# Kernel tuning notes

Measured on AMD Instinct MI355X. Metric: run time of the kernel, lower is better.

## Reference

```python
import jax, jax.numpy as jnp
import numpy as np


def setup_inputs() -> dict:
    key = jax.random.key(0)
    ks = jax.random.split(key, 8)
    B, Te, De, Dd, H = 64, 1024, 1024, 1024, 1024
    return {
        "encoder_outputs": jax.random.normal(ks[0], (B, Te, De), jnp.float32),
        "decoder_outputs": jax.random.normal(ks[1], (B, 1, Dd), jnp.float32),
        "Wa_w": jax.random.normal(ks[2], (H, Dd), jnp.float32) * 0.02,
        "Wa_b": jax.random.normal(ks[3], (H,), jnp.float32) * 0.02,
        "Ua_w": jax.random.normal(ks[4], (H, De), jnp.float32) * 0.02,
        "Ua_b": jax.random.normal(ks[5], (H,), jnp.float32) * 0.02,
        "Va_w": jax.random.normal(ks[6], (1, H), jnp.float32) * 0.02,
        "Va_b": jax.random.normal(ks[7], (1,), jnp.float32) * 0.02,
    }


def reference(encoder_outputs, decoder_outputs, Wa_w, Wa_b, Ua_w, Ua_b, Va_w, Va_b):
    # Wa: [B,1,H], Ua: [B,Te,H]  (torch Linear: x @ W.T + b)
    Wa = jnp.einsum('bqd,hd->bqh', decoder_outputs, Wa_w) + Wa_b
    Ua = jnp.einsum('bed,hd->beh', encoder_outputs, Ua_w) + Ua_b
    # broadcast add -> tanh -> scalar score per encoder position: [B,Te,1]
    scores = jnp.einsum('beh,oh->beo', jnp.tanh(Wa + Ua), Va_w) + Va_b
    scores = jnp.transpose(scores, (0, 2, 1))          # [B,1,Te]
    weights = jax.nn.softmax(scores, axis=-1)          # softmax over Te
    context = jnp.einsum('bqe,bed->bqd', weights, encoder_outputs)  # [B,1,De]
    return context
```

## Files before the change

kernel.cpp:

```cpp
#include <hip/hip_runtime.h>
#include <hip/hip_bf16.h>

#define B_  64
#define TE  1024
#define K_  1024
#define HH  1024
#define MM  (B_ * TE)

typedef __bf16 bf16x8 __attribute__((ext_vector_type(8)));
typedef __bf16 bf16x4 __attribute__((ext_vector_type(4)));
typedef float  f32x4  __attribute__((ext_vector_type(4)));

__device__ __forceinline__ float fast_tanh(float x) {
    float ax = __builtin_fabsf(x);
    float t  = __expf(-2.0f * ax);
    float r  = (1.0f - t) * __builtin_amdgcn_rcpf(1.0f + t);
    return __builtin_copysignf(r, x);
}

__global__ __launch_bounds__(256) void prep_kernel(const float* __restrict__ Ua_w,
                                                   __bf16* __restrict__ uawB,
                                                   const float* __restrict__ dec,
                                                   const float* __restrict__ Wa_w,
                                                   const float* __restrict__ Wa_b,
                                                   float* __restrict__ WaOut) {
    int bid = blockIdx.x, tid = threadIdx.x;
    if (bid < 256) {
        const long n4 = (long)HH * 1024 / 4;
        const float4* in4 = (const float4*)Ua_w;
        bf16x4* out4 = (bf16x4*)uawB;
        for (long j = bid * 256 + tid; j < n4; j += 65536) {
            float4 v = in4[j];
            bf16x4 o;
            o[0] = (__bf16)v.x; o[1] = (__bf16)v.y; o[2] = (__bf16)v.z; o[3] = (__bf16)v.w;
            out4[j] = o;
        }
        return;
    }
    int wb = bid - 256;
    int b = wb >> 4, hc = wb & 15;
    int wave = tid >> 6, lane = tid & 63;

    const float4* d4 = (const float4*)(dec + b * 1024);
    float4 dreg[4];
    #pragma unroll
    for (int j = 0; j < 4; j++) dreg[j] = d4[lane * 4 + j];

    #pragma unroll 4
    for (int i = 0; i < 16; i++) {
        int h = hc * 64 + wave * 16 + i;
        const float4* wr = (const float4*)(Wa_w + (long)h * 1024);
        float a = 0.0f;
        #pragma unroll
        for (int j = 0; j < 4; j++) {
            float4 v = wr[lane * 4 + j];
            a += v.x * dreg[j].x + v.y * dreg[j].y + v.z * dreg[j].z + v.w * dreg[j].w;
        }
        #pragma unroll
        for (int off = 32; off > 0; off >>= 1)
            a += __shfl_xor(a, off, 64);
        if (lane == 0) WaOut[b * 1024 + h] = a + Wa_b[h];
    }
}

#define MT 128
#define NP 256
#define KT 32
#define NSTEP (K_ / KT)
#define SWZ(r) (((r) >> 1) & 3)

__global__ __launch_bounds__(256, 2) void score_gemm(
    const float* __restrict__ Af,
    __bf16* __restrict__ encB,
    const __bf16* __restrict__ Bm,
    const float* __restrict__ Wa,
    const float* __restrict__ Ua_b,
    const float* __restrict__ Va_w,
    float* __restrict__ scores)
{
    __shared__ __bf16 sA[2][MT * KT];
    __shared__ __bf16 sB[2][NP * KT];
    __shared__ float sVa[NP];
    __shared__ float sWU[NP];

    const int tid  = threadIdx.x;
    const int wave = tid >> 6;
    const int lane = tid & 63;
    const int quad = lane >> 4;
    const int l16  = lane & 15;
    const int wm   = wave >> 1;
    const int wn   = wave & 1;

    const int bid = blockIdx.x;
    const int grp = bid >> 5;
    const int r5  = bid & 31;
    const int y   = r5 >> 3;
    const int x   = grp * 8 + (r5 & 7);

    const int rowBase = x * MT;
    const int colBase = y * NP;
    const int b       = rowBase >> 10;
    const bool wb     = (y == 0);

    if (tid < NP) {
        int h = colBase + tid;
        sVa[tid] = Va_w[h];
        sWU[tid] = Wa[b * 1024 + h] + Ua_b[h];
    }

    int rrA[2], sgA[2];
    #pragma unroll
    for (int i = 0; i < 2; i++) {
        int c = i * 256 + tid;
        rrA[i] = c >> 2;
        sgA[i] = (c & 3) ^ SWZ(rrA[i]);
    }

    const long aBase = (long)rowBase * K_;
    const long bBase = (long)colBase * K_;

    float4 pre[2][2];

    auto loadA = [&](int tk) {
        int k = tk * KT;
        #pragma unroll
        for (int i = 0; i < 2; i++) {
            const float4* p = (const float4*)(Af + aBase + (long)rrA[i] * K_ + k + sgA[i] * 8);
            pre[i][0] = p[0]; pre[i][1] = p[1];
        }
    };
    auto cvtA = [&](__bf16* sAn, int tk) {
        int k = tk * KT;
        #pragma unroll
        for (int i = 0; i < 2; i++) {
            bf16x8 v;
            v[0] = (__bf16)pre[i][0].x; v[1] = (__bf16)pre[i][0].y;
            v[2] = (__bf16)pre[i][0].z; v[3] = (__bf16)pre[i][0].w;
            v[4] = (__bf16)pre[i][1].x; v[5] = (__bf16)pre[i][1].y;
            v[6] = (__bf16)pre[i][1].z; v[7] = (__bf16)pre[i][1].w;
            *(bf16x8*)(sAn + (i * 256 + tid) * 8) = v;
            if (wb)
                *(bf16x8*)(encB + aBase + (long)rrA[i] * K_ + k + sgA[i] * 8) = v;
        }
    };
    auto stageB = [&](__bf16* sBn, int tk) {
        int k = tk * KT;
        #pragma unroll
        for (int i = 0; i < 4; i++) {
            int c = i * 256 + tid;
            int r = c >> 2;
            int seg = (c & 3) ^ SWZ(r);
            __builtin_amdgcn_global_load_lds(
                (const __attribute__((address_space(1))) unsigned int*)(Bm + bBase + (long)r * K_ + k + seg * 8),
                (__attribute__((address_space(3))) unsigned int*)(sBn + c * 8), 16, 0, 0);
        }
    };

    f32x4 acc[4][8] = {};

    auto compute = [&](const __bf16* sAc, const __bf16* sBc) {
        bf16x8 bfr[8];
        #pragma unroll
        for (int t8 = 0; t8 < 8; t8++) {
            int r = wn * 128 + t8 * 16 + l16;
            int slot = quad ^ SWZ(r);
            bfr[t8] = *(const bf16x8*)(sBc + r * KT + slot * 8);
        }
        #pragma unroll
        for (int s = 0; s < 4; s++) {
            int r = wm * 64 + s * 16 + l16;
            int slot = quad ^ SWZ(r);
            bf16x8 af = *(const bf16x8*)(sAc + r * KT + slot * 8);
            #pragma unroll
            for (int t8 = 0; t8 < 8; t8++)
                acc[s][t8] = __builtin_amdgcn_mfma_f32_16x16x32_bf16(af, bfr[t8], acc[s][t8], 0, 0, 0);
        }
    };

    loadA(0);
    stageB(sB[0], 0);
    cvtA(sA[0], 0);
    loadA(1);
    stageB(sB[1], 1);
    asm volatile("s_waitcnt vmcnt(8) lgkmcnt(0)" ::: "memory");
    __builtin_amdgcn_sched_barrier(0);
    __builtin_amdgcn_s_barrier();
    asm volatile("" ::: "memory");

    #pragma unroll 2
    for (int t = 0; t < NSTEP - 2; ++t) {
        const int cur = t & 1, nxt = cur ^ 1;
        compute(sA[cur], sB[cur]);
        cvtA(sA[nxt], t + 1);
        loadA(t + 2);
        asm volatile("s_waitcnt vmcnt(4) lgkmcnt(0)" ::: "memory");
        __builtin_amdgcn_sched_barrier(0);
        __builtin_amdgcn_s_barrier();
        asm volatile("" ::: "memory");
        stageB(sB[cur], t + 2);
    }
    {
        const int cur = (NSTEP - 2) & 1, nxt = cur ^ 1;
        compute(sA[cur], sB[cur]);
        cvtA(sA[nxt], NSTEP - 1);
        asm volatile("s_waitcnt vmcnt(0) lgkmcnt(0)" ::: "memory");
        __builtin_amdgcn_sched_barrier(0);
        __builtin_amdgcn_s_barrier();
        asm volatile("" ::: "memory");
    }
    compute(sA[(NSTEP - 1) & 1], sB[(NSTEP - 1) & 1]);

    float rs[4][4] = {};
    #pragma unroll
    for (int s = 0; s < 4; s++)
        #pragma unroll
        for (int t = 0; t < 8; t++) {
            int hl = wn * 128 + t * 16 + l16;
            float va = sVa[hl], wu = sWU[hl];
            #pragma unroll
            for (int r = 0; r < 4; r++)
                rs[s][r] += va * fast_tanh(acc[s][t][r] + wu);
        }

    #pragma unroll
    for (int s = 0; s < 4; s++)
        #pragma unroll
        for (int r = 0; r < 4; r++) {
            float v = rs[s][r];
            v += __shfl_xor(v, 1, 64);
            v += __shfl_xor(v, 2, 64);
            v += __shfl_xor(v, 4, 64);
            v += __shfl_xor(v, 8, 64);
            if (l16 == 0)
                atomicAdd(&scores[rowBase + wm * 64 + s * 16 + quad * 4 + r], v);
        }
}

__global__ __launch_bounds__(256) void softmax_kernel(float* __restrict__ s) {
    __shared__ float red[8];
    int b = blockIdx.x, tid = threadIdx.x;
    int wave = tid >> 6, lane = tid & 63;
    float4* row = (float4*)(s + b * 1024);
    float4 v = row[tid];
    float m = fmaxf(fmaxf(v.x, v.y), fmaxf(v.z, v.w));
    #pragma unroll
    for (int off = 32; off > 0; off >>= 1)
        m = fmaxf(m, __shfl_xor(m, off, 64));
    if (lane == 0) red[wave] = m;
    __syncthreads();
    m = fmaxf(fmaxf(red[0], red[1]), fmaxf(red[2], red[3]));
    v.x = expf(v.x - m); v.y = expf(v.y - m); v.z = expf(v.z - m); v.w = expf(v.w - m);
    float sum = v.x + v.y + v.z + v.w;
    #pragma unroll
    for (int off = 32; off > 0; off >>= 1)
        sum += __shfl_xor(sum, off, 64);
    if (lane == 0) red[4 + wave] = sum;
    __syncthreads();
    float inv = 1.0f / (red[4] + red[5] + red[6] + red[7]);
    v.x *= inv; v.y *= inv; v.z *= inv; v.w *= inv;
    row[tid] = v;
}

__global__ __launch_bounds__(256) void context_partial(const __bf16* __restrict__ enc,
                                                       const float* __restrict__ w,
                                                       float* __restrict__ pb) {
    __shared__ float red[2][128][8];
    int b = blockIdx.x, ec = blockIdx.y, tid = threadIdx.x;
    int eo = tid >> 7;
    int dc = tid & 127;
    const bf16x8* enc8 = (const bf16x8*)(enc + ((long)b * 1024 + ec * 128) * 1024);
    const float* wrow = w + b * 1024 + ec * 128;
    float acc[8] = {};
    #pragma unroll 4
    for (int e = eo; e < 128; e += 2) {
        float we = wrow[e];
        bf16x8 v = enc8[e * 128 + dc];
        #pragma unroll
        for (int j = 0; j < 8; j++) acc[j] += we * (float)v[j];
    }
    #pragma unroll
    for (int j = 0; j < 8; j++) red[eo][dc][j] = acc[j];
    __syncthreads();
    if (eo == 0) {
        float* o = pb + ((long)(b * 8 + ec)) * 1024 + dc * 8;
        #pragma unroll
        for (int j = 0; j < 8; j++) o[j] = red[0][dc][j] + red[1][dc][j];
    }
}

__global__ void context_reduce(const float* __restrict__ pb, float* __restrict__ out) {
    int b = blockIdx.x, tid = threadIdx.x;
    const f32x4* p4 = (const f32x4*)pb;
    f32x4 s = {0.f, 0.f, 0.f, 0.f};
    #pragma unroll
    for (int ec = 0; ec < 8; ec++)
        s += p4[(b * 8 + ec) * 256 + tid];
    ((f32x4*)out)[b * 256 + tid] = s;
}

extern "C" void kernel_launch(void* const* d_in, const int* in_sizes, int n_in,
                              void* d_out, int out_size, void* d_ws, size_t ws_size,
                              hipStream_t stream) {
    (void)in_sizes; (void)n_in; (void)ws_size;
    const float* enc   = (const float*)d_in[0];
    const float* dec   = (const float*)d_in[1];
    const float* Wa_w  = (const float*)d_in[2];
    const float* Wa_b  = (const float*)d_in[3];
    const float* Ua_w  = (const float*)d_in[4];
    const float* Ua_b  = (const float*)d_in[5];
    const float* Va_w  = (const float*)d_in[6];
    float* out = (float*)d_out;

    char* w = (char*)d_ws;
    __bf16* encB = (__bf16*)w;  w += (size_t)MM * 1024 * 2;
    __bf16* uawB = (__bf16*)w;  w += (size_t)HH * 1024 * 2;
    float* WaBuf = (float*)w;   w += (size_t)B_ * HH * 4;
    float* scores = (float*)w;  w += (size_t)MM * 4;
    float* pb = (float*)w;      w += (size_t)B_ * 8 * 1024 * 4;

    hipMemsetAsync(scores, 0, (size_t)MM * 4, stream);
    prep_kernel<<<dim3(256 + B_ * 16), 256, 0, stream>>>(Ua_w, uawB, dec, Wa_w, Wa_b, WaBuf);
    score_gemm<<<dim3((MM / MT) * (HH / NP)), 256, 0, stream>>>(enc, encB, uawB, WaBuf, Ua_b, Va_w, scores);
    softmax_kernel<<<dim3(B_), 256, 0, stream>>>(scores);
    context_partial<<<dim3(B_, 8), 256, 0, stream>>>(encB, scores, pb);
    context_reduce<<<dim3(B_), 256, 0, stream>>>(pb, out);
}
```

Baseline: 585.0 us.

## Restructure score GEMM with 512 threads, KT=64 and triple-buffered B staging

```diff
diff --git a/kernel.cpp b/kernel.cpp
--- a/kernel.cpp
+++ b/kernel.cpp
@@ -65,11 +65,11 @@
 
 #define MT 128
 #define NP 256
-#define KT 32
-#define NSTEP (K_ / KT)
-#define SWZ(r) (((r) >> 1) & 3)
-
-__global__ __launch_bounds__(256, 2) void score_gemm(
+#define KT 64
+#define NKT (K_ / KT)
+#define SMEM_SCORE (2 * MT * KT * 2 + 3 * NP * KT * 2 + 2 * NP * 4)
+
+__global__ __launch_bounds__(512, 2) void score_gemm(
     const float* __restrict__ Af,
     __bf16* __restrict__ encB,
     const __bf16* __restrict__ Bm,
@@ -78,18 +78,22 @@
     const float* __restrict__ Va_w,
     float* __restrict__ scores)
 {
-    __shared__ __bf16 sA[2][MT * KT];
-    __shared__ __bf16 sB[2][NP * KT];
-    __shared__ float sVa[NP];
-    __shared__ float sWU[NP];
+    extern __shared__ char smem[];
+    __bf16* aBuf0 = (__bf16*)smem;
+    __bf16* aBuf1 = aBuf0 + MT * KT;
+    __bf16* bBuf0 = (__bf16*)(smem + 2 * MT * KT * 2);
+    __bf16* bBuf1 = bBuf0 + NP * KT;
+    __bf16* bBuf2 = bBuf1 + NP * KT;
+    float*  sVa   = (float*)(smem + 2 * MT * KT * 2 + 3 * NP * KT * 2);
+    float*  sWU   = sVa + NP;
 
     const int tid  = threadIdx.x;
     const int wave = tid >> 6;
     const int lane = tid & 63;
     const int quad = lane >> 4;
     const int l16  = lane & 15;
-    const int wm   = wave >> 1;
-    const int wn   = wave & 1;
+    const int wr   = wave >> 2;
+    const int wc   = wave & 3;
 
     const int bid = blockIdx.x;
     const int grp = bid >> 5;
@@ -108,16 +112,16 @@
         sWU[tid] = Wa[b * 1024 + h] + Ua_b[h];
     }
 
-    int rrA[2], sgA[2];
-    #pragma unroll
-    for (int i = 0; i < 2; i++) {
-        int c = i * 256 + tid;
-        rrA[i] = c >> 2;
-        sgA[i] = (c & 3) ^ SWZ(rrA[i]);
-    }
-
     const long aBase = (long)rowBase * K_;
     const long bBase = (long)colBase * K_;
+
+    int rrA[2], sgA[2];
+    #pragma unroll
+    for (int i = 0; i < 2; i++) {
+        int c = i * 512 + tid;
+        rrA[i] = c >> 3;
+        sgA[i] = (c & 7) ^ (rrA[i] & 7);
+    }
 
     float4 pre[2][2];
 
@@ -129,7 +133,7 @@
             pre[i][0] = p[0]; pre[i][1] = p[1];
         }
     };
-    auto cvtA = [&](__bf16* sAn, int tk) {
+    auto cvtA = [&](__bf16* dst, int tk) {
         int k = tk * KT;
         #pragma unroll
         for (int i = 0; i < 2; i++) {
@@ -138,84 +142,105 @@
             v[2] = (__bf16)pre[i][0].z; v[3] = (__bf16)pre[i][0].w;
             v[4] = (__bf16)pre[i][1].x; v[5] = (__bf16)pre[i][1].y;
             v[6] = (__bf16)pre[i][1].z; v[7] = (__bf16)pre[i][1].w;
-            *(bf16x8*)(sAn + (i * 256 + tid) * 8) = v;
+            *(bf16x8*)(dst + (i * 512 + tid) * 8) = v;
             if (wb)
                 *(bf16x8*)(encB + aBase + (long)rrA[i] * K_ + k + sgA[i] * 8) = v;
         }
     };
-    auto stageB = [&](__bf16* sBn, int tk) {
+    auto stageB = [&](__bf16* dst, int tk) {
         int k = tk * KT;
         #pragma unroll
         for (int i = 0; i < 4; i++) {
-            int c = i * 256 + tid;
-            int r = c >> 2;
-            int seg = (c & 3) ^ SWZ(r);
+            int c = i * 512 + tid;
+            int r = c >> 3;
+            int seg = (c & 7) ^ (r & 7);
             __builtin_amdgcn_global_load_lds(
                 (const __attribute__((address_space(1))) unsigned int*)(Bm + bBase + (long)r * K_ + k + seg * 8),
-                (__attribute__((address_space(3))) unsigned int*)(sBn + c * 8), 16, 0, 0);
-        }
-    };
-
-    f32x4 acc[4][8] = {};
-
-    auto compute = [&](const __bf16* sAc, const __bf16* sBc) {
-        bf16x8 bfr[8];
-        #pragma unroll
-        for (int t8 = 0; t8 < 8; t8++) {
-            int r = wn * 128 + t8 * 16 + l16;
-            int slot = quad ^ SWZ(r);
-            bfr[t8] = *(const bf16x8*)(sBc + r * KT + slot * 8);
-        }
+                (__attribute__((address_space(3))) unsigned int*)(dst + c * 8), 16, 0, 0);
+        }
+    };
+
+    f32x4 acc[4][4] = {};
+    bf16x8 afr[4][2], bfr[4][2];
+
+    auto readFrags = [&](const __bf16* pa, const __bf16* pb) {
         #pragma unroll
         for (int s = 0; s < 4; s++) {
-            int r = wm * 64 + s * 16 + l16;
-            int slot = quad ^ SWZ(r);
-            bf16x8 af = *(const bf16x8*)(sAc + r * KT + slot * 8);
+            int r = wr * 64 + s * 16 + l16;
             #pragma unroll
-            for (int t8 = 0; t8 < 8; t8++)
-                acc[s][t8] = __builtin_amdgcn_mfma_f32_16x16x32_bf16(af, bfr[t8], acc[s][t8], 0, 0, 0);
-        }
-    };
+            for (int ks = 0; ks < 2; ks++) {
+                int slot = (ks * 4 + quad) ^ (r & 7);
+                afr[s][ks] = *(const bf16x8*)(pa + r * KT + slot * 8);
+            }
+        }
+        #pragma unroll
+        for (int t = 0; t < 4; t++) {
+            int r = wc * 64 + t * 16 + l16;
+            #pragma unroll
+            for (int ks = 0; ks < 2; ks++) {
+                int slot = (ks * 4 + quad) ^ (r & 7);
+                bfr[t][ks] = *(const bf16x8*)(pb + r * KT + slot * 8);
+            }
+        }
+    };
+    auto mfmaAll = [&]() {
+        __builtin_amdgcn_s_setprio(1);
+        #pragma unroll
+        for (int ks = 0; ks < 2; ks++)
+            #pragma unroll
+            for (int s = 0; s < 4; s++)
+                #pragma unroll
+                for (int t = 0; t < 4; t++)
+                    acc[s][t] = __builtin_amdgcn_mfma_f32_16x16x32_bf16(afr[s][ks], bfr[t][ks], acc[s][t], 0, 0, 0);
+        __builtin_amdgcn_s_setprio(0);
+    };
+
+    __bf16 *aCur = aBuf0, *aNxt = aBuf1;
+    __bf16 *bCur = bBuf0, *bNxt = bBuf1, *bStage = bBuf2;
 
     loadA(0);
-    stageB(sB[0], 0);
-    cvtA(sA[0], 0);
+    cvtA(aCur, 0);
+    stageB(bCur, 0);
     loadA(1);
-    stageB(sB[1], 1);
+    stageB(bNxt, 1);
     asm volatile("s_waitcnt vmcnt(8) lgkmcnt(0)" ::: "memory");
     __builtin_amdgcn_sched_barrier(0);
     __builtin_amdgcn_s_barrier();
     asm volatile("" ::: "memory");
 
-    #pragma unroll 2
-    for (int t = 0; t < NSTEP - 2; ++t) {
-        const int cur = t & 1, nxt = cur ^ 1;
-        compute(sA[cur], sB[cur]);
-        cvtA(sA[nxt], t + 1);
-        loadA(t + 2);
-        asm volatile("s_waitcnt vmcnt(4) lgkmcnt(0)" ::: "memory");
+    for (int kt = 0; kt < NKT - 2; ++kt) {
+        cvtA(aNxt, kt + 1);
+        loadA(kt + 2);
+        stageB(bStage, kt + 2);
+        readFrags(aCur, bCur);
+        asm volatile("s_waitcnt vmcnt(8) lgkmcnt(0)" ::: "memory");
         __builtin_amdgcn_sched_barrier(0);
         __builtin_amdgcn_s_barrier();
         asm volatile("" ::: "memory");
-        stageB(sB[cur], t + 2);
+        mfmaAll();
+        __bf16* ta = aCur; aCur = aNxt; aNxt = ta;
+        __bf16* tb = bCur; bCur = bNxt; bNxt = bStage; bStage = tb;
     }
     {
-        const int cur = (NSTEP - 2) & 1, nxt = cur ^ 1;
-        compute(sA[cur], sB[cur]);
-        cvtA(sA[nxt], NSTEP - 1);
+        cvtA(aNxt, NKT - 1);
+        readFrags(aCur, bCur);
         asm volatile("s_waitcnt vmcnt(0) lgkmcnt(0)" ::: "memory");
         __builtin_amdgcn_sched_barrier(0);
         __builtin_amdgcn_s_barrier();
         asm volatile("" ::: "memory");
-    }
-    compute(sA[(NSTEP - 1) & 1], sB[(NSTEP - 1) & 1]);
+        mfmaAll();
+        __bf16* ta = aCur; aCur = aNxt; aNxt = ta;
+        __bf16* tb = bCur; bCur = bNxt; bNxt = bStage; bStage = tb;
+    }
+    readFrags(aCur, bCur);
+    mfmaAll();
 
     float rs[4][4] = {};
     #pragma unroll
     for (int s = 0; s < 4; s++)
         #pragma unroll
-        for (int t = 0; t < 8; t++) {
-            int hl = wn * 128 + t * 16 + l16;
+        for (int t = 0; t < 4; t++) {
+            int hl = wc * 64 + t * 16 + l16;
             float va = sVa[hl], wu = sWU[hl];
             #pragma unroll
             for (int r = 0; r < 4; r++)
@@ -232,7 +257,7 @@
             v += __shfl_xor(v, 4, 64);
             v += __shfl_xor(v, 8, 64);
             if (l16 == 0)
-                atomicAdd(&scores[rowBase + wm * 64 + s * 16 + quad * 4 + r], v);
+                atomicAdd(&scores[rowBase + wr * 64 + s * 16 + quad * 4 + r], v);
         }
 }
 
@@ -318,9 +343,16 @@
     float* scores = (float*)w;  w += (size_t)MM * 4;
     float* pb = (float*)w;      w += (size_t)B_ * 8 * 1024 * 4;
 
+    static bool smemSet = false;
+    if (!smemSet) {
+        hipFuncSetAttribute((const void*)score_gemm,
+                            hipFuncAttributeMaxDynamicSharedMemorySize, SMEM_SCORE);
+        smemSet = true;
+    }
+
     hipMemsetAsync(scores, 0, (size_t)MM * 4, stream);
     prep_kernel<<<dim3(256 + B_ * 16), 256, 0, stream>>>(Ua_w, uawB, dec, Wa_w, Wa_b, WaBuf);
-    score_gemm<<<dim3((MM / MT) * (HH / NP)), 256, 0, stream>>>(enc, encB, uawB, WaBuf, Ua_b, Va_w, scores);
+    score_gemm<<<dim3((MM / MT) * (HH / NP)), 512, SMEM_SCORE, stream>>>(enc, encB, uawB, WaBuf, Ua_b, Va_w, scores);
     softmax_kernel<<<dim3(B_), 256, 0, stream>>>(scores);
     context_partial<<<dim3(B_, 8), 256, 0, stream>>>(encB, scores, pb);
     context_reduce<<<dim3(B_), 256, 0, stream>>>(pb, out);
```

Measured after the change: 586.9 us. About the same (+0.3%).
